# Kernel tuning notes

Measured on AMD Instinct MI355X. Metric: run time of the kernel, lower is better.

Reference implementation:

```python
import jax, jax.numpy as jnp
import numpy as np

B, N, K = 32, 8192, 256   # batch_size, mux_in, mux_out
TEMP = 1.0                # Gumbel-softmax temperature
MEM_PENALTY = -1000.0     # penalty for already-sampled elements


def setup_inputs() -> dict:
    key = jax.random.key(0)
    k1, k2 = jax.random.split(key)
    logits = jax.random.normal(k1, (B, N), dtype=jnp.float32)
    # Gumbel(0,1) noise, one draw per (batch, mux_in), repeated over mux_out
    u = jax.random.uniform(k2, (B, N), dtype=jnp.float32, minval=1e-6, maxval=1.0 - 1e-6)
    noise = -jnp.log(-jnp.log(u))
    sample_memory = jnp.zeros((B, N), dtype=jnp.float32)
    return {"logits": logits, "noise": noise, "sample_memory": sample_memory}


def reference(logits, noise, sample_memory):
    # perturbed logits, identical across the K (mux_out) axis -> keep as [B, N]
    perturbed = logits + noise + sample_memory * MEM_PENALTY  # [B, N]

    # top-K selection (straight-through hard path)
    _, topk_idx = jax.lax.top_k(perturbed, K)  # [B, K]
    b_idx = jnp.arange(B)[:, None]             # [B, 1]
    k_idx = jnp.arange(K)[None, :]             # [1, K]

    hard = jnp.zeros((B, N), logits.dtype).at[b_idx, topk_idx].set(1.0)
    hard = hard + sample_memory                # [B, N]

    # masking_matrix: for column k, all elements picked at steps < k are -inf,
    # the element picked at step k is 0 (scatter -inf, cumsum over k, reset to 0)
    M = jnp.zeros((B, N, K), logits.dtype).at[b_idx, topk_idx, k_idx].set(-jnp.inf)
    M = jnp.cumsum(M, axis=2)
    M = M.at[b_idx, topk_idx, k_idx].set(0.0)  # [B, N, K]

    masked = perturbed[:, :, None] + M                         # [B, N, K]
    soft = jax.nn.softmax(masked / TEMP, axis=1).sum(axis=2)   # [B, N]

    # straight-through estimator
    return hard - jax.lax.stop_gradient(soft) + soft
```

## Files before the change

### kernel.cpp

```cpp
#include <hip/hip_runtime.h>


#define BB 32
#define NN 8192
#define KK 256
#define THREADS 1024
#define EPT 8
#define NWAVE 16

__device__ __forceinline__ unsigned float_to_key(float f) {
    unsigned u = __float_as_uint(f);
    return (u & 0x80000000u) ? ~u : (u | 0x80000000u);
}

__global__ __launch_bounds__(THREADS) void topk_hard_kernel(
    const float* __restrict__ logits,
    const float* __restrict__ noise,
    const float* __restrict__ mem,
    float* __restrict__ out)
{
    __shared__ unsigned hist[NWAVE][256];
    __shared__ unsigned wpart[NWAVE];
    __shared__ unsigned sh_prefix, sh_need;

    const int tid  = threadIdx.x;
    const int wave = tid >> 6;
    const int lane = tid & 63;
    const int base = blockIdx.x * NN + tid * EPT;

    float4 lg0 = ((const float4*)(logits + base))[0];
    float4 lg1 = ((const float4*)(logits + base))[1];
    float4 no0 = ((const float4*)(noise  + base))[0];
    float4 no1 = ((const float4*)(noise  + base))[1];
    float4 mm0 = ((const float4*)(mem    + base))[0];
    float4 mm1 = ((const float4*)(mem    + base))[1];

    float p[EPT];
    p[0] = lg0.x + no0.x + mm0.x * -1000.0f;
    p[1] = lg0.y + no0.y + mm0.y * -1000.0f;
    p[2] = lg0.z + no0.z + mm0.z * -1000.0f;
    p[3] = lg0.w + no0.w + mm0.w * -1000.0f;
    p[4] = lg1.x + no1.x + mm1.x * -1000.0f;
    p[5] = lg1.y + no1.y + mm1.y * -1000.0f;
    p[6] = lg1.z + no1.z + mm1.z * -1000.0f;
    p[7] = lg1.w + no1.w + mm1.w * -1000.0f;

    unsigned key[EPT];
#pragma unroll
    for (int i = 0; i < EPT; ++i) key[i] = float_to_key(p[i]);

    unsigned need   = KK;
    unsigned prefix = 0;

#pragma unroll
    for (int level = 0; level < 4; ++level) {
        const int shift = 24 - 8 * level;

        if (level == 0) {
            ((uint4*)hist)[tid] = make_uint4(0u, 0u, 0u, 0u);
        } else if (tid < 64) {
            ((uint4*)hist)[tid] = make_uint4(0u, 0u, 0u, 0u);
        }
        __syncthreads();

        if (level == 0) {
            unsigned* h = hist[wave];
#pragma unroll
            for (int i = 0; i < EPT; ++i)
                atomicAdd(&h[key[i] >> 24], 1u);
        } else {
            const unsigned hi = prefix >> (shift + 8);
#pragma unroll
            for (int i = 0; i < EPT; ++i)
                if ((key[i] >> (shift + 8)) == hi)
                    atomicAdd(&hist[0][(key[i] >> shift) & 255u], 1u);
        }
        __syncthreads();

        unsigned c = 0, s = 0;
        if (tid < 256) {
            const int d = 255 - tid;
            if (level == 0) {
#pragma unroll
                for (int w = 0; w < NWAVE; ++w) c += hist[w][d];
            } else {
                c = hist[0][d];
            }
            s = c;
#pragma unroll
            for (int off = 1; off < 64; off <<= 1) {
                unsigned nv = __shfl_up(s, off, 64);
                if (lane >= off) s += nv;
            }
            if (lane == 63) wpart[wave] = s;
        }
        __syncthreads();
        if (tid < 256) {
            for (int w = 0; w < wave; ++w) s += wpart[w];
            const unsigned snext = s - c;
            if (s >= need && snext < need) {
                sh_prefix = prefix | ((unsigned)(255 - tid) << shift);
                sh_need   = need - snext;
            }
        }
        __syncthreads();
        prefix = sh_prefix;
        need   = sh_need;
    }

    const unsigned T = prefix;

    unsigned local_eq = 0;
#pragma unroll
    for (int i = 0; i < EPT; ++i) local_eq += (key[i] == T) ? 1u : 0u;

    unsigned s2 = local_eq;
#pragma unroll
    for (int off = 1; off < 64; off <<= 1) {
        unsigned nv = __shfl_up(s2, off, 64);
        if (lane >= off) s2 += nv;
    }
    if (lane == 63) wpart[wave] = s2;
    __syncthreads();
    unsigned radd = 0;
    for (int w = 0; w < wave; ++w) radd += wpart[w];
    unsigned rank = s2 - local_eq + radd;

    float o[EPT];
#pragma unroll
    for (int i = 0; i < EPT; ++i) {
        float sel;
        if (key[i] > T) {
            sel = 1.0f;
        } else if (key[i] == T) {
            sel = (rank < need) ? 1.0f : 0.0f;
            ++rank;
        } else {
            sel = 0.0f;
        }
        o[i] = sel;
    }
    o[0] += mm0.x; o[1] += mm0.y; o[2] += mm0.z; o[3] += mm0.w;
    o[4] += mm1.x; o[5] += mm1.y; o[6] += mm1.z; o[7] += mm1.w;

    ((float4*)(out + base))[0] = make_float4(o[0], o[1], o[2], o[3]);
    ((float4*)(out + base))[1] = make_float4(o[4], o[5], o[6], o[7]);
}

extern "C" void kernel_launch(void* const* d_in, const int* in_sizes, int n_in,
                              void* d_out, int out_size, void* d_ws, size_t ws_size,
                              hipStream_t stream) {
    const float* logits = (const float*)d_in[0];
    const float* noise  = (const float*)d_in[1];
    const float* mem    = (const float*)d_in[2];
    float* out = (float*)d_out;

    topk_hard_kernel<<<BB, THREADS, 0, stream>>>(logits, noise, mem, out);
}
```

Measured before the change: 65.32 us.

## Split top-k into two kernels with wider first-level histogram pass

```diff
diff --git a/kernel.cpp b/kernel.cpp
--- a/kernel.cpp
+++ b/kernel.cpp
@@ -1,32 +1,193 @@
 #include <hip/hip_runtime.h>
 
 
-#define BB 32
-#define NN 8192
-#define KK 256
-#define THREADS 1024
-#define EPT 8
-#define NWAVE 16
+#define NROW 32
+#define NCOL 8192
+#define KSEL 256
 
 __device__ __forceinline__ unsigned float_to_key(float f) {
     unsigned u = __float_as_uint(f);
     return (u & 0x80000000u) ? ~u : (u | 0x80000000u);
 }
 
-__global__ __launch_bounds__(THREADS) void topk_hard_kernel(
-    const float* __restrict__ logits,
-    const float* __restrict__ noise,
-    const float* __restrict__ mem,
+__global__ __launch_bounds__(256) void stage1(
+    const float* __restrict__ logits, const float* __restrict__ noise,
+    const float* __restrict__ mem, float* __restrict__ out,
+    unsigned* __restrict__ keys, unsigned* __restrict__ ghist)
+{
+    __shared__ __align__(16) unsigned h[4][256];
+    const int tid  = threadIdx.x;
+    const int wave = tid >> 6;
+    const int base = blockIdx.x * 1024 + tid * 4;
+
+    float4 lg = *(const float4*)(logits + base);
+    float4 no = *(const float4*)(noise  + base);
+    float4 mm = *(const float4*)(mem    + base);
+
+    ((uint4*)h)[tid] = make_uint4(0u, 0u, 0u, 0u);
+
+    unsigned k0 = float_to_key(lg.x + no.x + mm.x * -1000.0f);
+    unsigned k1 = float_to_key(lg.y + no.y + mm.y * -1000.0f);
+    unsigned k2 = float_to_key(lg.z + no.z + mm.z * -1000.0f);
+    unsigned k3 = float_to_key(lg.w + no.w + mm.w * -1000.0f);
+
+    *(float4*)(out  + base) = mm;
+    *(uint4*)(keys + base) = make_uint4(k0, k1, k2, k3);
+
+    __syncthreads();
+    unsigned* hw = h[wave];
+    atomicAdd(&hw[k0 >> 24], 1u);
+    atomicAdd(&hw[k1 >> 24], 1u);
+    atomicAdd(&hw[k2 >> 24], 1u);
+    atomicAdd(&hw[k3 >> 24], 1u);
+    __syncthreads();
+
+    ghist[blockIdx.x * 256 + tid] =
+        h[0][tid] + h[1][tid] + h[2][tid] + h[3][tid];
+}
+
+__device__ __forceinline__ void pick_digit(const unsigned* h, unsigned prefix,
+                                           unsigned need, int shift,
+                                           unsigned* sh_pn)
+{
+    const int lane = threadIdx.x & 63;
+    const int d0   = 255 - 4 * lane;
+    unsigned c0 = h[d0];
+    unsigned c1 = h[d0 - 1];
+    unsigned c2 = h[d0 - 2];
+    unsigned c3 = h[d0 - 3];
+    unsigned tot = c0 + c1 + c2 + c3;
+    unsigned s = tot;
+#pragma unroll
+    for (int off = 1; off < 64; off <<= 1) {
+        unsigned nv = __shfl_up(s, off, 64);
+        if (lane >= off) s += nv;
+    }
+    unsigned P    = s - tot;
+    unsigned cum0 = P + c0;
+    unsigned cum1 = cum0 + c1;
+    unsigned cum2 = cum1 + c2;
+    unsigned cum3 = cum2 + c3;
+    unsigned d = 0, nn = 0;
+    bool found = false;
+    if (cum0 >= need && P < need)          { d = (unsigned)d0;     nn = need - P;    found = true; }
+    else if (cum1 >= need && cum0 < need)  { d = (unsigned)d0 - 1; nn = need - cum0; found = true; }
+    else if (cum2 >= need && cum1 < need)  { d = (unsigned)d0 - 2; nn = need - cum1; found = true; }
+    else if (cum3 >= need && cum2 < need)  { d = (unsigned)d0 - 3; nn = need - cum2; found = true; }
+    if (found) {
+        sh_pn[0] = prefix | (d << shift);
+        sh_pn[1] = nn;
+    }
+}
+
+__global__ __launch_bounds__(1024) void stage2(
+    const unsigned* __restrict__ keys, const unsigned* __restrict__ ghist,
     float* __restrict__ out)
 {
-    __shared__ unsigned hist[NWAVE][256];
-    __shared__ unsigned wpart[NWAVE];
-    __shared__ unsigned sh_prefix, sh_need;
+    __shared__ __align__(16) unsigned hc[256];
+    __shared__ __align__(16) unsigned hA[256];
+    __shared__ __align__(16) unsigned hB[256];
+    __shared__ __align__(16) unsigned wpart[16];
+    __shared__ __align__(16) unsigned sh_pn[2];
 
     const int tid  = threadIdx.x;
     const int wave = tid >> 6;
     const int lane = tid & 63;
-    const int base = blockIdx.x * NN + tid * EPT;
+    const int base = blockIdx.x * NCOL + tid * 8;
+
+    uint4 ka = ((const uint4*)(keys + base))[0];
+    uint4 kb = ((const uint4*)(keys + base))[1];
+    unsigned key[8] = {ka.x, ka.y, ka.z, ka.w, kb.x, kb.y, kb.z, kb.w};
+
+    if (tid < 256) {
+        const unsigned* g = ghist + blockIdx.x * 8 * 256 + tid;
+        unsigned c = 0;
+#pragma unroll
+        for (int s = 0; s < 8; ++s) c += g[s * 256];
+        hc[tid] = c;
+    } else if (tid < 512) {
+        hA[tid - 256] = 0u;
+    }
+    __syncthreads();
+    if (wave == 0) pick_digit(hc, 0u, KSEL, 24, sh_pn);
+    __syncthreads();
+    unsigned prefix = sh_pn[0], need = sh_pn[1];
+
+    if (tid >= 256 && tid < 512) hB[tid - 256] = 0u;
+    {
+        const unsigned hi = prefix >> 24;
+#pragma unroll
+        for (int i = 0; i < 8; ++i)
+            if ((key[i] >> 24) == hi)
+                atomicAdd(&hA[(key[i] >> 16) & 255u], 1u);
+    }
+    __syncthreads();
+    if (wave == 0) pick_digit(hA, prefix, need, 16, sh_pn);
+    __syncthreads();
+    prefix = sh_pn[0]; need = sh_pn[1];
+
+    if (tid >= 256 && tid < 512) hA[tid - 256] = 0u;
+    {
+        const unsigned hi = prefix >> 16;
+#pragma unroll
+        for (int i = 0; i < 8; ++i)
+            if ((key[i] >> 16) == hi)
+                atomicAdd(&hB[(key[i] >> 8) & 255u], 1u);
+    }
+    __syncthreads();
+    if (wave == 0) pick_digit(hB, prefix, need, 8, sh_pn);
+    __syncthreads();
+    prefix = sh_pn[0]; need = sh_pn[1];
+
+    {
+        const unsigned hi = prefix >> 8;
+#pragma unroll
+        for (int i = 0; i < 8; ++i)
+            if ((key[i] >> 8) == hi)
+                atomicAdd(&hA[key[i] & 255u], 1u);
+    }
+    __syncthreads();
+    if (wave == 0) pick_digit(hA, prefix, need, 0, sh_pn);
+    __syncthreads();
+    const unsigned T     = sh_pn[0];
+    const unsigned needF = sh_pn[1];
+
+    unsigned local_eq = 0;
+#pragma unroll
+    for (int i = 0; i < 8; ++i) local_eq += (key[i] == T) ? 1u : 0u;
+    unsigned s2 = local_eq;
+#pragma unroll
+    for (int off = 1; off < 64; off <<= 1) {
+        unsigned nv = __shfl_up(s2, off, 64);
+        if (lane >= off) s2 += nv;
+    }
+    if (lane == 63) wpart[wave] = s2;
+    __syncthreads();
+    unsigned rank = s2 - local_eq;
+    for (int w = 0; w < wave; ++w) rank += wpart[w];
+
+#pragma unroll
+    for (int i = 0; i < 8; ++i) {
+        bool sel;
+        if (key[i] > T)       sel = true;
+        else if (key[i] == T) { sel = (rank < needF); ++rank; }
+        else                  sel = false;
+        if (sel) atomicAdd(out + base + i, 1.0f);
+    }
+}
+
+__global__ __launch_bounds__(1024) void topk_single(
+    const float* __restrict__ logits, const float* __restrict__ noise,
+    const float* __restrict__ mem, float* __restrict__ out)
+{
+    __shared__ __align__(16) unsigned hist[16][256];
+    __shared__ __align__(16) unsigned wpart[16];
+    __shared__ __align__(16) unsigned sh_pn[2];
+
+    const int tid  = threadIdx.x;
+    const int wave = tid >> 6;
+    const int lane = tid & 63;
+    const int base = blockIdx.x * NCOL + tid * 8;
 
     float4 lg0 = ((const float4*)(logits + base))[0];
     float4 lg1 = ((const float4*)(logits + base))[1];
@@ -35,85 +196,73 @@
     float4 mm0 = ((const float4*)(mem    + base))[0];
     float4 mm1 = ((const float4*)(mem    + base))[1];
 
-    float p[EPT];
-    p[0] = lg0.x + no0.x + mm0.x * -1000.0f;
-    p[1] = lg0.y + no0.y + mm0.y * -1000.0f;
-    p[2] = lg0.z + no0.z + mm0.z * -1000.0f;
-    p[3] = lg0.w + no0.w + mm0.w * -1000.0f;
-    p[4] = lg1.x + no1.x + mm1.x * -1000.0f;
-    p[5] = lg1.y + no1.y + mm1.y * -1000.0f;
-    p[6] = lg1.z + no1.z + mm1.z * -1000.0f;
-    p[7] = lg1.w + no1.w + mm1.w * -1000.0f;
-
-    unsigned key[EPT];
-#pragma unroll
-    for (int i = 0; i < EPT; ++i) key[i] = float_to_key(p[i]);
-
-    unsigned need   = KK;
-    unsigned prefix = 0;
-
+    unsigned key[8];
+    key[0] = float_to_key(lg0.x + no0.x + mm0.x * -1000.0f);
+    key[1] = float_to_key(lg0.y + no0.y + mm0.y * -1000.0f);
+    key[2] = float_to_key(lg0.z + no0.z + mm0.z * -1000.0f);
+    key[3] = float_to_key(lg0.w + no0.w + mm0.w * -1000.0f);
+    key[4] = float_to_key(lg1.x + no1.x + mm1.x * -1000.0f);
+    key[5] = float_to_key(lg1.y + no1.y + mm1.y * -1000.0f);
+    key[6] = float_to_key(lg1.z + no1.z + mm1.z * -1000.0f);
+    key[7] = float_to_key(lg1.w + no1.w + mm1.w * -1000.0f);
+
+    unsigned need = KSEL, prefix = 0;
 #pragma unroll
     for (int level = 0; level < 4; ++level) {
         const int shift = 24 - 8 * level;
-
-        if (level == 0) {
-            ((uint4*)hist)[tid] = make_uint4(0u, 0u, 0u, 0u);
-        } else if (tid < 64) {
-            ((uint4*)hist)[tid] = make_uint4(0u, 0u, 0u, 0u);
-        }
+        if (level == 0) { hist[tid >> 8][(tid & 255)] = 0u;
+                          hist[(tid >> 8) + 4][(tid & 255)] = 0u;
+                          hist[(tid >> 8) + 8][(tid & 255)] = 0u;
+                          hist[(tid >> 8) + 12][(tid & 255)] = 0u; }
+        else if (tid < 256) hist[0][tid] = 0u;
         __syncthreads();
-
         if (level == 0) {
             unsigned* h = hist[wave];
 #pragma unroll
-            for (int i = 0; i < EPT; ++i)
-                atomicAdd(&h[key[i] >> 24], 1u);
+            for (int i = 0; i < 8; ++i) atomicAdd(&h[key[i] >> 24], 1u);
         } else {
             const unsigned hi = prefix >> (shift + 8);
 #pragma unroll
-            for (int i = 0; i < EPT; ++i)
+            for (int i = 0; i < 8; ++i)
                 if ((key[i] >> (shift + 8)) == hi)
                     atomicAdd(&hist[0][(key[i] >> shift) & 255u], 1u);
         }
         __syncthreads();
-
-        unsigned c = 0, s = 0;
-        if (tid < 256) {
-            const int d = 255 - tid;
+        if (wave == 0) {
+            const int d0 = 255 - 4 * lane;
+            unsigned c0, c1, c2, c3;
             if (level == 0) {
-#pragma unroll
-                for (int w = 0; w < NWAVE; ++w) c += hist[w][d];
+                c0 = c1 = c2 = c3 = 0;
+#pragma unroll
+                for (int w = 0; w < 16; ++w) {
+                    c0 += hist[w][d0];     c1 += hist[w][d0 - 1];
+                    c2 += hist[w][d0 - 2]; c3 += hist[w][d0 - 3];
+                }
             } else {
-                c = hist[0][d];
+                c0 = hist[0][d0];     c1 = hist[0][d0 - 1];
+                c2 = hist[0][d0 - 2]; c3 = hist[0][d0 - 3];
             }
-            s = c;
+            unsigned tot = c0 + c1 + c2 + c3, s = tot;
 #pragma unroll
             for (int off = 1; off < 64; off <<= 1) {
                 unsigned nv = __shfl_up(s, off, 64);
                 if (lane >= off) s += nv;
             }
-            if (lane == 63) wpart[wave] = s;
+            unsigned P = s - tot;
+            unsigned cum0 = P + c0, cum1 = cum0 + c1, cum2 = cum1 + c2, cum3 = cum2 + c3;
+            if (cum0 >= need && P < need)         { sh_pn[0] = prefix | ((unsigned)d0 << shift);       sh_pn[1] = need - P; }
+            else if (cum1 >= need && cum0 < need) { sh_pn[0] = prefix | ((unsigned)(d0-1) << shift);   sh_pn[1] = need - cum0; }
+            else if (cum2 >= need && cum1 < need) { sh_pn[0] = prefix | ((unsigned)(d0-2) << shift);   sh_pn[1] = need - cum1; }
+            else if (cum3 >= need && cum2 < need) { sh_pn[0] = prefix | ((unsigned)(d0-3) << shift);   sh_pn[1] = need - cum2; }
         }
         __syncthreads();
-        if (tid < 256) {
-            for (int w = 0; w < wave; ++w) s += wpart[w];
-            const unsigned snext = s - c;
-            if (s >= need && snext < need) {
-                sh_prefix = prefix | ((unsigned)(255 - tid) << shift);
-                sh_need   = need - snext;
-            }
-        }
-        __syncthreads();
-        prefix = sh_prefix;
-        need   = sh_need;
-    }
-
-    const unsigned T = prefix;
+        prefix = sh_pn[0]; need = sh_pn[1];
+    }
+    const unsigned T = prefix, needF = need;
 
     unsigned local_eq = 0;
 #pragma unroll
-    for (int i = 0; i < EPT; ++i) local_eq += (key[i] == T) ? 1u : 0u;
-
+    for (int i = 0; i < 8; ++i) local_eq += (key[i] == T) ? 1u : 0u;
     unsigned s2 = local_eq;
 #pragma unroll
     for (int off = 1; off < 64; off <<= 1) {
@@ -122,27 +271,20 @@
     }
     if (lane == 63) wpart[wave] = s2;
     __syncthreads();
-    unsigned radd = 0;
-    for (int w = 0; w < wave; ++w) radd += wpart[w];
-    unsigned rank = s2 - local_eq + radd;
-
-    float o[EPT];
-#pragma unroll
-    for (int i = 0; i < EPT; ++i) {
+    unsigned rank = s2 - local_eq;
+    for (int w = 0; w < wave; ++w) rank += wpart[w];
+
+    float o[8];
+#pragma unroll
+    for (int i = 0; i < 8; ++i) {
         float sel;
-        if (key[i] > T) {
-            sel = 1.0f;
-        } else if (key[i] == T) {
-            sel = (rank < need) ? 1.0f : 0.0f;
-            ++rank;
-        } else {
-            sel = 0.0f;
-        }
+        if (key[i] > T)       sel = 1.0f;
+        else if (key[i] == T) { sel = (rank < needF) ? 1.0f : 0.0f; ++rank; }
+        else                  sel = 0.0f;
         o[i] = sel;
     }
     o[0] += mm0.x; o[1] += mm0.y; o[2] += mm0.z; o[3] += mm0.w;
     o[4] += mm1.x; o[5] += mm1.y; o[6] += mm1.z; o[7] += mm1.w;
-
     ((float4*)(out + base))[0] = make_float4(o[0], o[1], o[2], o[3]);
     ((float4*)(out + base))[1] = make_float4(o[4], o[5], o[6], o[7]);
 }
@@ -155,5 +297,15 @@
     const float* mem    = (const float*)d_in[2];
     float* out = (float*)d_out;
 
-    topk_hard_kernel<<<BB, THREADS, 0, stream>>>(logits, noise, mem, out);
-}
+    const size_t keys_bytes  = (size_t)NROW * NCOL * sizeof(unsigned);
+    const size_t ghist_bytes = (size_t)256 * 256 * sizeof(unsigned);
+
+    if (ws_size >= keys_bytes + ghist_bytes) {
+        unsigned* keys  = (unsigned*)d_ws;
+        unsigned* ghist = (unsigned*)((char*)d_ws + keys_bytes);
+        stage1<<<256, 256, 0, stream>>>(logits, noise, mem, out, keys, ghist);
+        stage2<<<NROW, 1024, 0, stream>>>(keys, ghist, out);
+    } else {
+        topk_single<<<NROW, 1024, 0, stream>>>(logits, noise, mem, out);
+    }
+}
```

Result: no change. 64.75 us (-0.9%).
